# Kernel tuning notes

Measured on AMD Instinct MI355X. Metric: run time of the kernel, lower is better.

Reference implementation:

```python
import jax, jax.numpy as jnp
import numpy as np

_SQRT_2_OVER_PI = 0.7978845608028654  # sqrt(2/pi)
_EPS = 1e-12  # F.normalize default eps


def _gelu_tanh(x):
    return 0.5 * x * (1.0 + jnp.tanh(_SQRT_2_OVER_PI * (x + 0.044715 * x * x * x)))


def _l2_normalize(v):
    n = jnp.linalg.norm(v, axis=-1, keepdims=True)
    return v / jnp.maximum(n, _EPS)


def setup_inputs() -> dict:
    key = jax.random.key(0)
    k_x, k_p = jax.random.split(key)
    B, T, D, K = 4, 4096, 4096, 256
    x = jax.random.normal(k_x, (B, T, D), dtype=jnp.float32)
    emas = jax.random.normal(k_p, (K, D), dtype=jnp.float32)
    log_tau = jnp.asarray(np.log(2.0), dtype=jnp.float32)           # GELU2_TEMP
    log_blend = jnp.asarray(np.log(0.3 / 0.7), dtype=jnp.float32)   # GELU2_BLEND logit
    logit_decay = jnp.asarray(np.log(0.9 / 0.1), dtype=jnp.float32) # GELU2_EMA_DECAY logit
    return {"x": x, "emas": emas, "log_tau": log_tau,
            "log_blend": log_blend, "logit_decay": logit_decay}


def reference(x, emas, log_tau, log_blend, logit_decay):
    # Steady-state (_ready=True) forward of GELU2.
    tau = jnp.exp(log_tau)
    alpha = jax.nn.sigmoid(log_blend)
    d = jax.nn.sigmoid(logit_decay)

    x_norm = _l2_normalize(x)          # (B,T,D)
    p_norm = _l2_normalize(emas)       # (K,D)
    sim = jnp.einsum('btd,kd->btk', x_norm, p_norm)  # (B,T,K)
    max_sim = jnp.max(sim, axis=-1)    # (B,T)
    novelty = jnp.exp(-tau * max_sim)  # (B,T)
    scale = 1.0 - alpha * d + alpha * d * novelty[..., None]  # (B,T,1)
    out = _gelu_tanh(x * scale)

    # Competitive EMA prototype update (detached, stateful in torch).
    x_mean = jnp.mean(x.reshape(-1, x.shape[-1]), axis=0)        # (D,)
    x_mean_n = _l2_normalize(x_mean[None, :])                    # (1,D)
    k_star = jnp.argmax(jnp.sum(p_norm * x_mean_n, axis=-1))     # scalar
    d_val = jax.lax.stop_gradient(d)
    new_row = d_val * emas[k_star] + (1.0 - d_val) * jax.lax.stop_gradient(x_mean)
    new_emas = emas.at[k_star].set(new_row)

    return out, new_emas
```

## Files before the change

### kernel.cpp

```cpp
#include <hip/hip_runtime.h>
#include <hip/hip_bf16.h>

typedef __bf16 bf16x8 __attribute__((ext_vector_type(8)));
typedef float  f32x4  __attribute__((ext_vector_type(4)));

#define N_ROWS 16384
#define DDIM   4096
#define KPROT  256
#define BM     32
#define BK     64
#define OUT0_ELEMS 67108864

#define WS_PB    0
#define WS_INV   2097152
#define WS_CSUM  2098176
#define WS_CELL  2114560

__device__ __forceinline__ unsigned f2bf2(float lo, float hi) {
    unsigned a = __float_as_uint(lo), b = __float_as_uint(hi);
    a = (a + 0x7FFFu + ((a >> 16) & 1u)) >> 16;
    b = (b + 0x7FFFu + ((b >> 16) & 1u)) >> 16;
    return a | (b << 16);
}

__device__ __forceinline__ float gelu_tanh(float y) {
    float z = 0.7978845608028654f * (y + 0.044715f * y * y * y);
    float t = __expf(2.f * z);
    float th = 1.f - __fdividef(2.f, t + 1.f);
    return 0.5f * y * (1.f + th);
}

__device__ __forceinline__ float sigmoidf(float v) {
    return 1.f / (1.f + __expf(-v));
}

__global__ void __launch_bounds__(256) prep_kernel(const float* __restrict__ emas,
                                                   unsigned* __restrict__ pb,
                                                   float* __restrict__ inv_norm) {
    const int k = blockIdx.x, t = threadIdx.x;
    const int lane = t & 63, w = t >> 6;
    const f32x4* er = (const f32x4*)(emas + (size_t)k * DDIM);
    f32x4 v[4];
    float ss = 0.f;
#pragma unroll
    for (int j = 0; j < 4; ++j) {
        v[j] = er[j * 256 + t];
        ss += v[j][0] * v[j][0] + v[j][1] * v[j][1] + v[j][2] * v[j][2] + v[j][3] * v[j][3];
    }
#pragma unroll
    for (int m = 1; m < 64; m <<= 1) ss += __shfl_xor(ss, m);
    __shared__ float red[4];
    if (lane == 0) red[w] = ss;
    __syncthreads();
    float tot = red[0] + red[1] + red[2] + red[3];
    float inv = 1.f / fmaxf(sqrtf(tot), 1e-12f);
    if (t == 0) inv_norm[k] = inv;
#pragma unroll
    for (int j = 0; j < 4; ++j) {
        uint2 p2;
        p2.x = f2bf2(v[j][0] * inv, v[j][1] * inv);
        p2.y = f2bf2(v[j][2] * inv, v[j][3] * inv);
        *(uint2*)(pb + (size_t)k * 2048 + (size_t)(j * 256 + t) * 2) = p2;
    }
}

__global__ void __launch_bounds__(256, 2)
main_kernel(const float* __restrict__ x, const unsigned* __restrict__ pb,
            const float* __restrict__ log_tau, const float* __restrict__ log_blend,
            const float* __restrict__ logit_decay,
            float* __restrict__ outp, float* __restrict__ colsum) {
    __shared__ __align__(16) unsigned lds_a[8 * BM * 4];
    __shared__ __align__(16) unsigned lds_b[8 * KPROT * 4];
    __shared__ float lds_wmax[4][BM];
    __shared__ float lds_sumsq[BM];
    __shared__ float lds_scale[BM];

    const int t = threadIdx.x;
    const int lane = t & 63, w = t >> 6;
    const int q = lane >> 4, rr = lane & 15;
    const int arow = t >> 3, ac = t & 7;
    const size_t row0 = (size_t)blockIdx.x * BM;

    const f32x4 zero = {0.f, 0.f, 0.f, 0.f};
    f32x4 acc[2][4];
#pragma unroll
    for (int rt = 0; rt < 2; ++rt)
#pragma unroll
        for (int ct = 0; ct < 4; ++ct) acc[rt][ct] = zero;

    float ss = 0.f;
    const float* xrow = x + (row0 + (size_t)arow) * DDIM + ac * 4;

    for (int it = 0; it < DDIM / BK; ++it) {
        const int k0 = it * BK;
        f32x4 va = __builtin_nontemporal_load((const f32x4*)(xrow + k0));
        f32x4 vb = __builtin_nontemporal_load((const f32x4*)(xrow + k0 + 32));
        ss += va[0] * va[0] + va[1] * va[1] + va[2] * va[2] + va[3] * va[3];
        ss += vb[0] * vb[0] + vb[1] * vb[1] + vb[2] * vb[2] + vb[3] * vb[3];
        uint2 pa, pbv;
        pa.x = f2bf2(va[0], va[1]);  pa.y = f2bf2(va[2], va[3]);
        pbv.x = f2bf2(vb[0], vb[1]); pbv.y = f2bf2(vb[2], vb[3]);
        *(uint2*)&lds_a[(ac >> 1) * 128 + arow * 4 + (ac & 1) * 2] = pa;
        *(uint2*)&lds_a[((ac >> 1) + 4) * 128 + arow * 4 + (ac & 1) * 2] = pbv;
#pragma unroll
        for (int i = 0; i < 8; ++i) {
            const int n = arow + i * 32;
            int4 g = *(const int4*)(pb + (size_t)n * 2048 + (k0 >> 1) + ac * 4);
            *(int4*)&lds_b[ac * 1024 + n * 4] = g;
        }
        __syncthreads();
#pragma unroll
        for (int ks8 = 0; ks8 < 8; ks8 += 4) {
            const int kcq = ks8 + q;
            bf16x8 af[2], bfr[4];
            af[0] = *(const bf16x8*)&lds_a[kcq * 128 + rr * 4];
            af[1] = *(const bf16x8*)&lds_a[kcq * 128 + (16 + rr) * 4];
#pragma unroll
            for (int ct = 0; ct < 4; ++ct)
                bfr[ct] = *(const bf16x8*)&lds_b[kcq * 1024 + (w * 64 + ct * 16 + rr) * 4];
#pragma unroll
            for (int rt = 0; rt < 2; ++rt)
#pragma unroll
                for (int ct = 0; ct < 4; ++ct)
                    acc[rt][ct] = __builtin_amdgcn_mfma_f32_16x16x32_bf16(
                        af[rt], bfr[ct], acc[rt][ct], 0, 0, 0);
        }
        __syncthreads();
    }

    ss += __shfl_xor(ss, 1); ss += __shfl_xor(ss, 2); ss += __shfl_xor(ss, 4);
    if (ac == 0) lds_sumsq[arow] = ss;

#pragma unroll
    for (int rt = 0; rt < 2; ++rt)
#pragma unroll
        for (int i = 0; i < 4; ++i) {
            float m = fmaxf(fmaxf(acc[rt][0][i], acc[rt][1][i]),
                            fmaxf(acc[rt][2][i], acc[rt][3][i]));
            m = fmaxf(m, __shfl_xor(m, 1));
            m = fmaxf(m, __shfl_xor(m, 2));
            m = fmaxf(m, __shfl_xor(m, 4));
            m = fmaxf(m, __shfl_xor(m, 8));
            if (rr == 0) lds_wmax[w][rt * 16 + q * 4 + i] = m;
        }
    __syncthreads();

    if (t < BM) {
        float m = fmaxf(fmaxf(lds_wmax[0][t], lds_wmax[1][t]),
                        fmaxf(lds_wmax[2][t], lds_wmax[3][t]));
        float nrm = fmaxf(sqrtf(lds_sumsq[t]), 1e-12f);
        float msim = m / nrm;
        float tau = __expf(log_tau[0]);
        float ad = sigmoidf(log_blend[0]) * sigmoidf(logit_decay[0]);
        lds_scale[t] = 1.f - ad + ad * __expf(-tau * msim);
    }
    __syncthreads();

    float cs[4][4];
#pragma unroll
    for (int j = 0; j < 4; ++j)
#pragma unroll
        for (int e = 0; e < 4; ++e) cs[j][e] = 0.f;

    for (int r = 0; r < BM; ++r) {
        const float s = lds_scale[r];
        const f32x4* xr = (const f32x4*)(x + (row0 + (size_t)r) * DDIM);
        f32x4* orow = (f32x4*)(outp + (row0 + (size_t)r) * DDIM);
#pragma unroll
        for (int j = 0; j < 4; ++j) {
            f32x4 v = __builtin_nontemporal_load(&xr[j * 256 + t]);
            cs[j][0] += v[0]; cs[j][1] += v[1]; cs[j][2] += v[2]; cs[j][3] += v[3];
            f32x4 g;
            g[0] = gelu_tanh(v[0] * s); g[1] = gelu_tanh(v[1] * s);
            g[2] = gelu_tanh(v[2] * s); g[3] = gelu_tanh(v[3] * s);
            __builtin_nontemporal_store(g, &orow[j * 256 + t]);
        }
    }
#pragma unroll
    for (int j = 0; j < 4; ++j)
#pragma unroll
        for (int e = 0; e < 4; ++e)
            atomicAdd(&colsum[j * 1024 + t * 4 + e], cs[j][e]);
}

__global__ void __launch_bounds__(256) argmax_kernel(const float* __restrict__ emas,
                                                     const float* __restrict__ colsum,
                                                     const float* __restrict__ inv_norm,
                                                     unsigned long long* __restrict__ cell) {
    const int k = blockIdx.x, t = threadIdx.x;
    const int lane = t & 63, w = t >> 6;
    const f32x4* er = (const f32x4*)(emas + (size_t)k * DDIM);
    const f32x4* cr = (const f32x4*)colsum;
    float s = 0.f;
#pragma unroll
    for (int j = 0; j < 4; ++j) {
        f32x4 a = er[j * 256 + t], b = cr[j * 256 + t];
        s += a[0] * b[0] + a[1] * b[1] + a[2] * b[2] + a[3] * b[3];
    }
#pragma unroll
    for (int m = 1; m < 64; m <<= 1) s += __shfl_xor(s, m);
    __shared__ float red[4];
    if (lane == 0) red[w] = s;
    __syncthreads();
    if (t == 0) {
        float dotv = (red[0] + red[1] + red[2] + red[3]) * inv_norm[k];
        unsigned u = __float_as_uint(dotv);
        unsigned key = (u & 0x80000000u) ? ~u : (u | 0x80000000u);
        unsigned long long pk = ((unsigned long long)key << 32) |
                                (unsigned long long)(unsigned)(~k);
        atomicMax(cell, pk);
    }
}

__global__ void __launch_bounds__(256) final_kernel(const float* __restrict__ emas,
                                                    const float* __restrict__ colsum,
                                                    const unsigned long long* __restrict__ cell,
                                                    const float* __restrict__ logit_decay,
                                                    float* __restrict__ out2) {
    const int idx = blockIdx.x * 256 + threadIdx.x;
    const int e = idx * 4;
    const int k = e >> 12, d0 = e & 4095;
    f32x4 v = *(const f32x4*)(emas + e);
    const unsigned kstar = ~(unsigned)(*cell);
    if ((unsigned)k == kstar) {
        const float dd = sigmoidf(logit_decay[0]);
        const float od = (1.f - dd) * (1.f / 16384.f);
        f32x4 xm = *(const f32x4*)(colsum + d0);
        v[0] = dd * v[0] + od * xm[0];
        v[1] = dd * v[1] + od * xm[1];
        v[2] = dd * v[2] + od * xm[2];
        v[3] = dd * v[3] + od * xm[3];
    }
    *(f32x4*)(out2 + e) = v;
}

extern "C" void kernel_launch(void* const* d_in, const int* in_sizes, int n_in,
                              void* d_out, int out_size, void* d_ws, size_t ws_size,
                              hipStream_t stream) {
    const float* x           = (const float*)d_in[0];
    const float* emas        = (const float*)d_in[1];
    const float* log_tau     = (const float*)d_in[2];
    const float* log_blend   = (const float*)d_in[3];
    const float* logit_decay = (const float*)d_in[4];
    float* outp     = (float*)d_out;
    float* out_emas = outp + (size_t)OUT0_ELEMS;

    char* ws = (char*)d_ws;
    unsigned* pb                 = (unsigned*)(ws + WS_PB);
    float* inv_norm              = (float*)(ws + WS_INV);
    float* colsum                = (float*)(ws + WS_CSUM);
    unsigned long long* cell     = (unsigned long long*)(ws + WS_CELL);

    (void)hipMemsetAsync(colsum, 0, 16384 + 8, stream);

    prep_kernel<<<KPROT, 256, 0, stream>>>(emas, pb, inv_norm);
    main_kernel<<<N_ROWS / BM, 256, 0, stream>>>(x, pb, log_tau, log_blend,
                                                 logit_decay, outp, colsum);
    argmax_kernel<<<KPROT, 256, 0, stream>>>(emas, colsum, inv_norm, cell);
    final_kernel<<<KPROT * DDIM / 1024, 256, 0, stream>>>(emas, colsum, cell,
                                                          logit_decay, out_emas);
}
```

Measured before the change: 646.7 us.

## Register-prefetch next K tile and XOR-swizzle LDS layout for A/B tiles

Global loads of the next x and prototype tiles are issued into registers right after the barrier, so they overlap with the MFMA work on the current tile instead of stalling at the loop top. LDS writes and reads for both operand tiles are XOR-swizzled by the k-chunk index to cut bank conflicts. This raises register pressure through the 8 int4 prefetch registers plus the x vectors, which could lower occupancy.

New measurement: 850.3 us. 1.31x slower.

```diff
diff --git a/kernel.cpp b/kernel.cpp
--- a/kernel.cpp
+++ b/kernel.cpp
@@ -90,34 +90,49 @@
 
     float ss = 0.f;
     const float* xrow = x + (row0 + (size_t)arow) * DDIM + ac * 4;
+    const unsigned* pbbase = pb + (size_t)arow * 2048 + ac * 4;
+
+    f32x4 va = __builtin_nontemporal_load((const f32x4*)(xrow));
+    f32x4 vb = __builtin_nontemporal_load((const f32x4*)(xrow + 32));
+    int4 gb[8];
+#pragma unroll
+    for (int i = 0; i < 8; ++i)
+        gb[i] = *(const int4*)(pbbase + (size_t)i * 65536);
 
     for (int it = 0; it < DDIM / BK; ++it) {
-        const int k0 = it * BK;
-        f32x4 va = __builtin_nontemporal_load((const f32x4*)(xrow + k0));
-        f32x4 vb = __builtin_nontemporal_load((const f32x4*)(xrow + k0 + 32));
         ss += va[0] * va[0] + va[1] * va[1] + va[2] * va[2] + va[3] * va[3];
         ss += vb[0] * vb[0] + vb[1] * vb[1] + vb[2] * vb[2] + vb[3] * vb[3];
         uint2 pa, pbv;
         pa.x = f2bf2(va[0], va[1]);  pa.y = f2bf2(va[2], va[3]);
         pbv.x = f2bf2(vb[0], vb[1]); pbv.y = f2bf2(vb[2], vb[3]);
-        *(uint2*)&lds_a[(ac >> 1) * 128 + arow * 4 + (ac & 1) * 2] = pa;
-        *(uint2*)&lds_a[((ac >> 1) + 4) * 128 + arow * 4 + (ac & 1) * 2] = pbv;
+        const int kca = ac >> 1, kcb = kca + 4;
+        *(uint2*)&lds_a[kca * 128 + ((arow ^ kca) * 4) + (ac & 1) * 2] = pa;
+        *(uint2*)&lds_a[kcb * 128 + ((arow ^ kcb) * 4) + (ac & 1) * 2] = pbv;
 #pragma unroll
         for (int i = 0; i < 8; ++i) {
             const int n = arow + i * 32;
-            int4 g = *(const int4*)(pb + (size_t)n * 2048 + (k0 >> 1) + ac * 4);
-            *(int4*)&lds_b[ac * 1024 + n * 4] = g;
+            *(int4*)&lds_b[ac * 1024 + ((n ^ ac) * 4)] = gb[i];
         }
         __syncthreads();
+        if (it + 1 < DDIM / BK) {
+            const int k0n = (it + 1) * BK;
+            va = __builtin_nontemporal_load((const f32x4*)(xrow + k0n));
+            vb = __builtin_nontemporal_load((const f32x4*)(xrow + k0n + 32));
+#pragma unroll
+            for (int i = 0; i < 8; ++i)
+                gb[i] = *(const int4*)(pbbase + (size_t)i * 65536 + (it + 1) * 32);
+        }
 #pragma unroll
         for (int ks8 = 0; ks8 < 8; ks8 += 4) {
             const int kcq = ks8 + q;
             bf16x8 af[2], bfr[4];
-            af[0] = *(const bf16x8*)&lds_a[kcq * 128 + rr * 4];
-            af[1] = *(const bf16x8*)&lds_a[kcq * 128 + (16 + rr) * 4];
-#pragma unroll
-            for (int ct = 0; ct < 4; ++ct)
-                bfr[ct] = *(const bf16x8*)&lds_b[kcq * 1024 + (w * 64 + ct * 16 + rr) * 4];
+            af[0] = *(const bf16x8*)&lds_a[kcq * 128 + ((rr ^ kcq) * 4)];
+            af[1] = *(const bf16x8*)&lds_a[kcq * 128 + (((16 + rr) ^ kcq) * 4)];
+#pragma unroll
+            for (int ct = 0; ct < 4; ++ct) {
+                const int n = w * 64 + ct * 16 + rr;
+                bfr[ct] = *(const bf16x8*)&lds_b[kcq * 1024 + ((n ^ kcq) * 4)];
+            }
 #pragma unroll
             for (int rt = 0; rt < 2; ++rt)
 #pragma unroll
```
